# Kernel optimization log

Measured on AMD Instinct MI355X. Metric: run time of the kernel, lower is better.

The kernel has to match this reference:

```python
import jax, jax.numpy as jnp
import numpy as np

B, W, M, H, L, C, LR, RD = 128, 64, 512, 64, 2, 4, 16, 32
D = L * H  # concatenated GRU hidden dim


def setup_inputs() -> dict:
    key = jax.random.key(0)
    ks = jax.random.split(key, 22)
    def rn(k, shape, s=0.1):
        return jax.random.normal(k, shape, jnp.float32) * s
    return dict(
        x=jax.random.normal(ks[0], (B, W, M), jnp.float32),
        H_init=rn(ks[1], (L, M, H)),
        major_graph=rn(ks[2], (M, M), 0.05),
        wx0=rn(ks[3], (3 * H, 1)), wh0=rn(ks[4], (3 * H, H)),
        bx0=rn(ks[5], (3 * H,)), bh0=rn(ks[6], (3 * H,)),
        wx1=rn(ks[7], (3 * H, H)), wh1=rn(ks[8], (3 * H, H)),
        bx1=rn(ks[9], (3 * H,)), bh1=rn(ks[10], (3 * H,)),
        A_v=rn(ks[11], (C, LR, M)), A_g=1.0 + rn(ks[12], (C, LR)), A_b=rn(ks[13], (C, LR)),
        B_v=rn(ks[14], (C, M, LR)), B_g=1.0 + rn(ks[15], (C, M)), B_b=rn(ks[16], (C, M)),
        C_v=rn(ks[17], (C, RD, D)), C_g=1.0 + rn(ks[18], (C, RD)), C_b=rn(ks[19], (C, RD)),
        FR_w=rn(ks[20], (C, M, RD)), FR_b=rn(ks[21], (C, M)),
    )


def _wn(v, g):
    # weight_norm: W = g * v / ||v|| per output row (norm over input dim)
    return g[..., None] * v / jnp.linalg.norm(v, axis=-1, keepdims=True)


def _gru(x, h, wx, wh, bx, bh):
    gx = x @ wx.T + bx            # [B, M, 3H]
    gh = h @ wh.T + bh            # [B, M, 3H]
    xr, xz, xn = jnp.split(gx, 3, axis=-1)
    hr, hz, hn = jnp.split(gh, 3, axis=-1)
    r = jax.nn.sigmoid(xr + hr)
    z = jax.nn.sigmoid(xz + hz)
    n = jnp.tanh(xn + r * hn)
    return n + z * (h - n)


def reference(x, H_init, major_graph, wx0, wh0, bx0, bh0, wx1, wh1, bx1, bh1,
              A_v, A_g, A_b, B_v, B_g, B_b, C_v, C_g, C_b, FR_w, FR_b):
    Bsz = x.shape[0]
    Aw = _wn(A_v, A_g)            # [C, LR, M]
    Bw = _wn(B_v, B_g)            # [C, M, LR]
    Cw = _wn(C_v, C_g)            # [C, RD, D]
    # h0: [L, B, M, H]
    h0 = jnp.broadcast_to(H_init[:, None], (H_init.shape[0], Bsz) + H_init.shape[1:])
    h0_1 = h0[1]

    def step(hn, x_t):
        # NOTE: faithfully, layer0 receives the top layer's hidden from the
        # previous step; layer1 always uses the fixed h0[1].
        h1 = _gru(x_t[..., None], hn, wx0, wh0, bx0, bh0)   # [B, M, H]
        h2 = _gru(h1, h0_1, wx1, wh1, bx1, bh1)             # [B, M, H]
        x_p = jnp.swapaxes(jnp.concatenate([h1, h2], axis=-1), 1, 2)  # [B, D, M]
        x_p0 = jax.nn.relu(x_p @ major_graph)               # [B, D, M]
        a = jnp.einsum('bdm,clm->bcdl', x_p, Aw) + A_b[:, None, :]      # [B,C,D,LR]
        bmid = jnp.einsum('bcdl,cml->bcdm', a, Bw) + B_b[:, None, :]    # [B,C,D,M]
        xr = jax.nn.relu(bmid + x_p0[:, None])              # [B, C, D, M]
        xt = jnp.swapaxes(xr, 2, 3)                         # [B, C, M, D]
        y = jax.nn.sigmoid(jnp.einsum('bcmd,crd->bcmr', xt, Cw) + C_b[:, None, :])
        out = jnp.einsum('bcmr,cmr->bcm', y, FR_w) + FR_b   # [B, C, M]
        return h2, out

    _, outs = jax.lax.scan(step, h0[0], jnp.moveaxis(x, 1, 0))  # [W, B, C, M]
    final = jnp.transpose(outs, (2, 1, 0, 3))                   # [C, B, W, M]
    return final.reshape((-1,) + final.shape[2:])               # [C*B, W, M]
```

## Files before the change

### kernel.cpp

```cpp
#include <hip/hip_runtime.h>
#include <hip/hip_bf16.h>

constexpr int kB  = 128;
constexpr int kW  = 64;
constexpr int kM  = 512;
constexpr int kH  = 64;
constexpr int kC  = 4;
constexpr int kLR = 16;
constexpr int kRD = 32;
constexpr int kD  = 128;
constexpr int kNC = kB * kM;
constexpr int kN  = kM + kC * kLR;

typedef __attribute__((ext_vector_type(8))) short bf16x8;
typedef __attribute__((ext_vector_type(4))) float f32x4;

__device__ __forceinline__ float sigmf(float v) { return 1.f / (1.f + __expf(-v)); }
__device__ __forceinline__ float tanhf2(float v) { float e = __expf(2.f * v); return 1.f - 2.f / (e + 1.f); }

__device__ __forceinline__ unsigned short f2bfu(float f) {
    union { __hip_bfloat16 h; unsigned short u; } cv; cv.h = __float2bfloat16(f); return cv.u;
}
__device__ __forceinline__ float bfu2f(unsigned short s) {
    return __uint_as_float(((unsigned)s) << 16);
}

__device__ __forceinline__ void gl_lds16(const void* g, void* s) {
    __builtin_amdgcn_global_load_lds(
        (const __attribute__((address_space(1))) void*)(g),
        (__attribute__((address_space(3))) void*)(s), 16, 0, 0);
}


__global__ void k_initHc(const float* __restrict__ Hini, __hip_bfloat16* __restrict__ HcG) {
    int id = blockIdx.x * 256 + threadIdx.x;
    int cell = id >> 6, j = id & 63;
    int m = cell & (kM - 1);
    HcG[id] = __float2bfloat16(Hini[m * kH + j]);
}

__global__ void k_h1b(const float* __restrict__ Hini, __hip_bfloat16* __restrict__ H1b) {
    int id = blockIdx.x * 256 + threadIdx.x;
    H1b[id] = __float2bfloat16(Hini[(kM + (id >> 6)) * kH + (id & 63)]);
}

__global__ void k_gh1T(const float* __restrict__ Hini, const float* __restrict__ wh1,
                       const float* __restrict__ bh1, float* __restrict__ gh1T) {
    int id = blockIdx.x * 256 + threadIdx.x;
    int k = id >> 9, m = id & (kM - 1);
    float acc = bh1[k];
    #pragma unroll
    for (int j = 0; j < kH; j++)
        acc = fmaf(Hini[(kM + m) * kH + j], wh1[k * kH + j], acc);
    gh1T[id] = acc;
}

__global__ void k_packW(const float* __restrict__ wh0, const float* __restrict__ wx1,
                        __hip_bfloat16* __restrict__ W0g, __hip_bfloat16* __restrict__ W1x) {
    int id = blockIdx.x * 256 + threadIdx.x;
    W0g[id] = __float2bfloat16(wh0[id]);
    W1x[id] = __float2bfloat16(wx1[id]);
}

__global__ void k_buildGT(const float* __restrict__ G, __hip_bfloat16* __restrict__ BT) {
    int id = blockIdx.x * 256 + threadIdx.x;
    int n = id >> 9, k = id & (kM - 1);
    BT[n * kM + k] = __float2bfloat16(G[k * kM + n]);
}

__global__ void k_norm_aw(const float* __restrict__ Av, const float* __restrict__ Ag,
                          __hip_bfloat16* __restrict__ BT) {
    int row = blockIdx.x;
    int lane = threadIdx.x;
    float v[8]; float s = 0.f;
    #pragma unroll
    for (int q = 0; q < 8; q++) { v[q] = Av[row * kM + q * 64 + lane]; s += v[q] * v[q]; }
    #pragma unroll
    for (int off = 32; off > 0; off >>= 1) s += __shfl_down(s, off);
    s = __shfl(s, 0);
    float scale = Ag[row] / sqrtf(s);
    #pragma unroll
    for (int q = 0; q < 8; q++)
        BT[(kM + row) * kM + q * 64 + lane] = __float2bfloat16(v[q] * scale);
}

__global__ void k_norm_bw(const float* __restrict__ Bv, const float* __restrict__ Bg,
                          const float* __restrict__ Bb, __hip_bfloat16* __restrict__ BwNh) {
    int row = blockIdx.x * 256 + threadIdx.x;
    float v[16]; float s = 0.f;
    #pragma unroll
    for (int l = 0; l < 16; l++) { v[l] = Bv[row * 16 + l]; s += v[l] * v[l]; }
    float scale = Bg[row] / sqrtf(s);
    #pragma unroll
    for (int l = 0; l < 16; l++) BwNh[row * 32 + l] = __float2bfloat16(v[l] * scale);
    BwNh[row * 32 + 16] = __float2bfloat16(Bb[row]);
    #pragma unroll
    for (int l = 17; l < 32; l++) BwNh[row * 32 + l] = __float2bfloat16(0.f);
}

__global__ void k_norm_cw(const float* __restrict__ Cv, const float* __restrict__ Cg,
                          __hip_bfloat16* __restrict__ CwB) {
    int row = blockIdx.x;
    int lane = threadIdx.x;
    float v0 = Cv[row * kD + lane], v1 = Cv[row * kD + 64 + lane];
    float s = v0 * v0 + v1 * v1;
    #pragma unroll
    for (int off = 32; off > 0; off >>= 1) s += __shfl_down(s, off);
    s = __shfl(s, 0);
    float scale = Cg[row] / sqrtf(s);
    CwB[row * kD + lane] = __float2bfloat16(v0 * scale);
    CwB[row * kD + 64 + lane] = __float2bfloat16(v1 * scale);
}

__global__ __launch_bounds__(512) void k_gru(
    const float* __restrict__ x,
    __hip_bfloat16* __restrict__ HcG,
    const __hip_bfloat16* __restrict__ H1b,
    const __hip_bfloat16* __restrict__ W0g,
    const __hip_bfloat16* __restrict__ W1x,
    const float* __restrict__ gh1T,
    const float* __restrict__ wx0, const float* __restrict__ bx0,
    const float* __restrict__ bh0, const float* __restrict__ bx1,
    __hip_bfloat16* __restrict__ XPT, int t)
{
    __shared__ __align__(16) short W0s[192 * 64];
    __shared__ __align__(16) short W1s[192 * 64];
    __shared__ __align__(16) short HlS[128 * 64];
    __shared__ float xsh[128];

    const int tid = threadIdx.x;
    const int blk = blockIdx.x;
    const int w = tid >> 6, lane = tid & 63;
    const int lr = lane & 15, lq = lane >> 4;
    const int b = blk >> 2;
    const int mBlk = (blk & 3) * 128;
    const unsigned short* HcU = (const unsigned short*)HcG;
    const unsigned short* H1U = (const unsigned short*)H1b;
    const size_t cellBase = (size_t)blk * 128;

    #pragma unroll
    for (int it = 0; it < 3; it++) {
        int cid = it * 512 + tid; int row = cid >> 3, c = cid & 7;
        gl_lds16(W0g + row * 64 + ((c ^ (row & 7)) * 8), W0s + cid * 8);
    }
    #pragma unroll
    for (int it = 0; it < 3; it++) {
        int cid = it * 512 + tid; int row = cid >> 3, c = cid & 7;
        gl_lds16(W1x + row * 64 + ((c ^ (row & 7)) * 8), W1s + cid * 8);
    }
    if (tid < 128) xsh[tid] = x[((size_t)b * kW + t) * kM + mBlk + tid];
    __syncthreads();

    const int cl = w * 16 + lr;

    bf16x8 a0[2];
    a0[0] = *(const bf16x8*)&HcU[(cellBase + cl) * 64 + lq * 8];
    a0[1] = *(const bf16x8*)&HcU[(cellBase + cl) * 64 + (4 + lq) * 8];
    f32x4 aR[4] = {}, aZ[4] = {}, aN[4] = {};
    #pragma unroll
    for (int kc = 0; kc < 2; kc++) {
        #pragma unroll
        for (int gt = 0; gt < 4; gt++) {
            const int gR = gt * 16 + lr;
            const int gZ = 64 + gt * 16 + lr;
            const int gN = 128 + gt * 16 + lr;
            bf16x8 bR = *(const bf16x8*)&W0s[gR * 64 + (((kc * 4 + lq) ^ (gR & 7)) * 8)];
            bf16x8 bZ = *(const bf16x8*)&W0s[gZ * 64 + (((kc * 4 + lq) ^ (gZ & 7)) * 8)];
            bf16x8 bN = *(const bf16x8*)&W0s[gN * 64 + (((kc * 4 + lq) ^ (gN & 7)) * 8)];
            aR[gt] = __builtin_amdgcn_mfma_f32_16x16x32_bf16(a0[kc], bR, aR[gt], 0, 0, 0);
            aZ[gt] = __builtin_amdgcn_mfma_f32_16x16x32_bf16(a0[kc], bZ, aZ[gt], 0, 0, 0);
            aN[gt] = __builtin_amdgcn_mfma_f32_16x16x32_bf16(a0[kc], bN, aN[gt], 0, 0, 0);
        }
    }

    #pragma unroll
    for (int gt = 0; gt < 4; gt++) {
        const int i = gt * 16 + lr;
        const float wxr = wx0[i], wxz = wx0[64 + i], wxn = wx0[128 + i];
        const float bsr = bx0[i] + bh0[i];
        const float bsz = bx0[64 + i] + bh0[64 + i];
        const float bxn = bx0[128 + i], bhn = bh0[128 + i];
        unsigned short hu[4];
        #pragma unroll
        for (int r2 = 0; r2 < 4; r2++) {
            const int clr = w * 16 + lq * 4 + r2;
            const float xv = xsh[clr];
            float rr = sigmf(aR[gt][r2] + bsr + xv * wxr);
            float zz = sigmf(aZ[gt][r2] + bsz + xv * wxz);
            float nn = tanhf2(bxn + xv * wxn + rr * (aN[gt][r2] + bhn));
            float hp = bfu2f(HcU[(cellBase + clr) * 64 + i]);
            float h1 = nn + zz * (hp - nn);
            unsigned short u = f2bfu(h1);
            HlS[clr * 64 + (((i >> 3) ^ (clr & 7)) * 8) + (i & 7)] = (short)u;
            hu[r2] = u;
        }
        ushort4 pk; pk.x = hu[0]; pk.y = hu[1]; pk.z = hu[2]; pk.w = hu[3];
        *(ushort4*)((unsigned short*)XPT + (size_t)(b * 128 + i) * kM + mBlk + w * 16 + lq * 4) = pk;
    }

    bf16x8 a1[2];
    a1[0] = *(const bf16x8*)&HlS[cl * 64 + ((lq ^ (cl & 7)) * 8)];
    a1[1] = *(const bf16x8*)&HlS[cl * 64 + (((4 + lq) ^ (cl & 7)) * 8)];
    f32x4 cR[4] = {}, cZ[4] = {}, cN[4] = {};
    #pragma unroll
    for (int kc = 0; kc < 2; kc++) {
        #pragma unroll
        for (int gt = 0; gt < 4; gt++) {
            const int gR = gt * 16 + lr;
            const int gZ = 64 + gt * 16 + lr;
            const int gN = 128 + gt * 16 + lr;
            bf16x8 bR = *(const bf16x8*)&W1s[gR * 64 + (((kc * 4 + lq) ^ (gR & 7)) * 8)];
            bf16x8 bZ = *(const bf16x8*)&W1s[gZ * 64 + (((kc * 4 + lq) ^ (gZ & 7)) * 8)];
            bf16x8 bN = *(const bf16x8*)&W1s[gN * 64 + (((kc * 4 + lq) ^ (gN & 7)) * 8)];
            cR[gt] = __builtin_amdgcn_mfma_f32_16x16x32_bf16(a1[kc], bR, cR[gt], 0, 0, 0);
            cZ[gt] = __builtin_amdgcn_mfma_f32_16x16x32_bf16(a1[kc], bZ, cZ[gt], 0, 0, 0);
            cN[gt] = __builtin_amdgcn_mfma_f32_16x16x32_bf16(a1[kc], bN, cN[gt], 0, 0, 0);
        }
    }

    const int mb4 = mBlk + w * 16 + lq * 4;
    #pragma unroll
    for (int gt = 0; gt < 4; gt++) {
        const int i = gt * 16 + lr;
        const float bxr = bx1[i], bxz = bx1[64 + i], bxn = bx1[128 + i];
        f32x4 gr4 = *(const f32x4*)&gh1T[(size_t)i * kM + mb4];
        f32x4 gz4 = *(const f32x4*)&gh1T[(size_t)(64 + i) * kM + mb4];
        f32x4 gn4 = *(const f32x4*)&gh1T[(size_t)(128 + i) * kM + mb4];
        unsigned short hu[4];
        #pragma unroll
        for (int r2 = 0; r2 < 4; r2++) {
            const int clr = w * 16 + lq * 4 + r2;
            float rr = sigmf(cR[gt][r2] + bxr + gr4[r2]);
            float zz = sigmf(cZ[gt][r2] + bxz + gz4[r2]);
            float nn = tanhf2(cN[gt][r2] + bxn + rr * gn4[r2]);
            float h01 = bfu2f(H1U[(size_t)(mBlk + clr) * 64 + i]);
            float h2 = nn + zz * (h01 - nn);
            unsigned short u = f2bfu(h2);
            hu[r2] = u;
            ((unsigned short*)HcG)[(cellBase + clr) * 64 + i] = u;
        }
        ushort4 pk; pk.x = hu[0]; pk.y = hu[1]; pk.z = hu[2]; pk.w = hu[3];
        *(ushort4*)((unsigned short*)XPT + (size_t)(b * 128 + 64 + i) * kM + mBlk + w * 16 + lq * 4) = pk;
    }
}

__global__ __launch_bounds__(256) void k_tail(
    const __hip_bfloat16* __restrict__ X,
    const __hip_bfloat16* __restrict__ BT,
    const float* __restrict__ Ab,
    const __hip_bfloat16* __restrict__ BwNh,
    const __hip_bfloat16* __restrict__ CwB,
    const float* __restrict__ Cb, const float* __restrict__ FRw,
    const float* __restrict__ FRb, float* __restrict__ OUT, int t)
{
    __shared__ __align__(16) short SM[40960];
    short* xp0L = SM;
    short* aL   = SM + 8192;
    short* Xr   = SM + 32768;

    const int tid = threadIdx.x;
    const int b = blockIdx.x, mseg = blockIdx.y;
    const int w = tid >> 6, lane = tid & 63;
    const int lr = lane & 15, lq = lane >> 4;
    const int wm = w >> 1, wn = w & 1;

    f32x4 acc[4][4] = {};
    const __hip_bfloat16* Xb = X + (size_t)b * 128 * kM;

    auto STAGE = [&](int kk, int buf) {
        short* AsB = SM + buf * 16384;
        short* BsB = AsB + 8192;
        #pragma unroll
        for (int it = 0; it < 4; it++) {
            int cid = it * 256 + tid;
            int row = cid >> 3, ch = cid & 7;
            int cg = ch ^ (row & 7);
            gl_lds16(Xb + (size_t)row * kM + kk + cg * 8, AsB + cid * 8);
        }
        #pragma unroll
        for (int it = 0; it < 4; it++) {
            int cid = it * 256 + tid;
            int j = cid >> 3, ch = cid & 7;
            int cg = ch ^ (j & 7);
            int n = (j < 64) ? (mseg * 64 + j) : (448 + j);
            gl_lds16(BT + (size_t)n * kM + kk + cg * 8, BsB + cid * 8);
        }
    };

    STAGE(0, 0);
    __syncthreads();

    int cur = 0;
    for (int ki = 0; ki < 8; ki++) {
        if (ki < 7) STAGE((ki + 1) * 64, cur ^ 1);
        const short* AsB = SM + cur * 16384;
        const short* BsB = AsB + 8192;
        #pragma unroll
        for (int w2 = 0; w2 < 2; w2++) {
            bf16x8 af[4], bfr[4];
            #pragma unroll
            for (int fi = 0; fi < 4; fi++) {
                int row = wm * 64 + fi * 16 + lr;
                af[fi] = *(const bf16x8*)&AsB[row * 64 + (((w2 * 4 + lq) ^ (row & 7)) * 8)];
            }
            #pragma unroll
            for (int fj = 0; fj < 4; fj++) {
                int col = wn * 64 + fj * 16 + lr;
                bfr[fj] = *(const bf16x8*)&BsB[col * 64 + (((w2 * 4 + lq) ^ (col & 7)) * 8)];
            }
            #pragma unroll
            for (int fi = 0; fi < 4; fi++)
                #pragma unroll
                for (int fj = 0; fj < 4; fj++)
                    acc[fi][fj] = __builtin_amdgcn_mfma_f32_16x16x32_bf16(
                        af[fi], bfr[fj], acc[fi][fj], 0, 0, 0);
        }
        __syncthreads();
        cur ^= 1;
    }

    if (wn == 0) {
        #pragma unroll
        for (int fi = 0; fi < 4; fi++) {
            const int d0 = wm * 64 + fi * 16 + lq * 4;
            const int c16 = d0 >> 3, half = lq & 1;
            #pragma unroll
            for (int fj = 0; fj < 4; fj++) {
                const int ml = fj * 16 + lr;
                unsigned lo = (unsigned)f2bfu(fmaxf(acc[fi][fj][0], 0.f)) |
                              ((unsigned)f2bfu(fmaxf(acc[fi][fj][1], 0.f)) << 16);
                unsigned hi = (unsigned)f2bfu(fmaxf(acc[fi][fj][2], 0.f)) |
                              ((unsigned)f2bfu(fmaxf(acc[fi][fj][3], 0.f)) << 16);
                uint2 pk; pk.x = lo; pk.y = hi;
                *(uint2*)&xp0L[ml * 128 + ((c16 ^ (ml & 7)) * 8) + half * 4] = pk;
            }
        }
    } else {
        #pragma unroll
        for (int fj = 0; fj < 4; fj++) {
            const int clc = fj * 16 + lr;
            const float ab = Ab[clc];
            #pragma unroll
            for (int fi = 0; fi < 4; fi++) {
                #pragma unroll
                for (int r = 0; r < 4; r++) {
                    const int d = wm * 64 + fi * 16 + lq * 4 + r;
                    aL[d * 64 + (((clc >> 3) ^ (d & 7)) * 8) + (clc & 7)] =
                        (short)f2bfu(acc[fi][fj][r] + ab);
                }
            }
        }
    }
    __syncthreads();

    const int c = w;
    bf16x8 af2[8];
    #pragma unroll
    for (int dt = 0; dt < 8; dt++) {
        bf16x8 v = {};
        const int d = dt * 16 + lr;
        if (lq < 2) {
            v = *(const bf16x8*)&aL[d * 64 + (((c * 2 + lq) ^ (d & 7)) * 8)];
        } else if (lq == 2) {
            v[0] = (short)0x3F80;
        }
        af2[dt] = v;
    }
    bf16x8 cwf[2][4];
    #pragma unroll
    for (int rt = 0; rt < 2; rt++)
        #pragma unroll
        for (int s = 0; s < 4; s++)
            cwf[rt][s] = *(const bf16x8*)&CwB[((size_t)(c * kRD + rt * 16 + lr)) * kD + s * 32 + lq * 8];
    const float cbv0 = Cb[c * kRD + lr];
    const float cbv1 = Cb[c * kRD + 16 + lr];
    short* Xrw = Xr + w * 2048;

    for (int mt = 0; mt < 4; mt++) {
        const int mg = mseg * 64 + mt * 16 + lr;
        bf16x8 bf1 = *(const bf16x8*)&BwNh[((size_t)c * kM + mg) * 32 + lq * 8];
        f32x4 acc1[8] = {};
        #pragma unroll
        for (int dt = 0; dt < 8; dt++)
            acc1[dt] = __builtin_amdgcn_mfma_f32_16x16x32_bf16(af2[dt], bf1, acc1[dt], 0, 0, 0);

        const int mlT = mt * 16 + lr;
        #pragma unroll
        for (int dt = 0; dt < 8; dt++) {
            const int c16 = dt * 2 + (lq >> 1), half = lq & 1;
            uint2 xv = *(const uint2*)&xp0L[mlT * 128 + ((c16 ^ (mlT & 7)) * 8) + half * 4];
            float x0 = bfu2f((unsigned short)(xv.x & 0xFFFF));
            float x1 = bfu2f((unsigned short)(xv.x >> 16));
            float x2 = bfu2f((unsigned short)(xv.y & 0xFFFF));
            float x3 = bfu2f((unsigned short)(xv.y >> 16));
            unsigned lo = (unsigned)f2bfu(fmaxf(acc1[dt][0] + x0, 0.f)) |
                          ((unsigned)f2bfu(fmaxf(acc1[dt][1] + x1, 0.f)) << 16);
            unsigned hi = (unsigned)f2bfu(fmaxf(acc1[dt][2] + x2, 0.f)) |
                          ((unsigned)f2bfu(fmaxf(acc1[dt][3] + x3, 0.f)) << 16);
            uint2 pk; pk.x = lo; pk.y = hi;
            *(uint2*)&Xrw[lr * 128 + ((c16 ^ (lr & 7)) * 8) + half * 4] = pk;
        }

        bf16x8 xa[4];
        #pragma unroll
        for (int s = 0; s < 4; s++)
            xa[s] = *(const bf16x8*)&Xrw[lr * 128 + (((s * 4 + lq) ^ (lr & 7)) * 8)];
        float po0 = 0.f, po1 = 0.f, po2 = 0.f, po3 = 0.f;
        const int mrow = mseg * 64 + mt * 16 + lq * 4;
        #pragma unroll
        for (int rt = 0; rt < 2; rt++) {
            f32x4 a2 = {};
            #pragma unroll
            for (int s = 0; s < 4; s++)
                a2 = __builtin_amdgcn_mfma_f32_16x16x32_bf16(xa[s], cwf[rt][s], a2, 0, 0, 0);
            const float cb = rt ? cbv1 : cbv0;
            const int r = rt * 16 + lr;
            po0 = fmaf(sigmf(a2[0] + cb), FRw[((size_t)c * kM + mrow + 0) * kRD + r], po0);
            po1 = fmaf(sigmf(a2[1] + cb), FRw[((size_t)c * kM + mrow + 1) * kRD + r], po1);
            po2 = fmaf(sigmf(a2[2] + cb), FRw[((size_t)c * kM + mrow + 2) * kRD + r], po2);
            po3 = fmaf(sigmf(a2[3] + cb), FRw[((size_t)c * kM + mrow + 3) * kRD + r], po3);
        }
        #pragma unroll
        for (int off = 8; off > 0; off >>= 1) {
            po0 += __shfl_xor(po0, off);
            po1 += __shfl_xor(po1, off);
            po2 += __shfl_xor(po2, off);
            po3 += __shfl_xor(po3, off);
        }
        if (lr == 0) {
            const float* frb = &FRb[c * kM + mrow];
            float4 o;
            o.x = po0 + frb[0]; o.y = po1 + frb[1];
            o.z = po2 + frb[2]; o.w = po3 + frb[3];
            *(float4*)&OUT[((size_t)(c * kB + b) * kW + t) * kM + mrow] = o;
        }
    }
}

extern "C" void kernel_launch(void* const* d_in, const int* in_sizes, int n_in,
                              void* d_out, int out_size, void* d_ws, size_t ws_size,
                              hipStream_t stream) {
    const float* x    = (const float*)d_in[0];
    const float* Hini = (const float*)d_in[1];
    const float* G    = (const float*)d_in[2];
    const float* wx0  = (const float*)d_in[3];
    const float* wh0  = (const float*)d_in[4];
    const float* bx0  = (const float*)d_in[5];
    const float* bh0  = (const float*)d_in[6];
    const float* wx1  = (const float*)d_in[7];
    const float* wh1  = (const float*)d_in[8];
    const float* bx1  = (const float*)d_in[9];
    const float* bh1  = (const float*)d_in[10];
    const float* A_v  = (const float*)d_in[11];
    const float* A_g  = (const float*)d_in[12];
    const float* A_b  = (const float*)d_in[13];
    const float* B_v  = (const float*)d_in[14];
    const float* B_g  = (const float*)d_in[15];
    const float* B_b  = (const float*)d_in[16];
    const float* C_v  = (const float*)d_in[17];
    const float* C_g  = (const float*)d_in[18];
    const float* C_b  = (const float*)d_in[19];
    const float* FR_w = (const float*)d_in[20];
    const float* FR_b = (const float*)d_in[21];
    float* out = (float*)d_out;

    char* w = (char*)d_ws;
    __hip_bfloat16* HcG  = (__hip_bfloat16*)w; w += (size_t)kNC * 64 * 2;
    __hip_bfloat16* XPT  = (__hip_bfloat16*)w; w += (size_t)128 * kNC * 2;
    __hip_bfloat16* BT   = (__hip_bfloat16*)w; w += (size_t)kN * kM * 2;
    __hip_bfloat16* H1b  = (__hip_bfloat16*)w; w += (size_t)kM * kH * 2;
    __hip_bfloat16* W0g  = (__hip_bfloat16*)w; w += (size_t)192 * 64 * 2;
    __hip_bfloat16* W1xg = (__hip_bfloat16*)w; w += (size_t)192 * 64 * 2;
    float*          gh1T = (float*)w;          w += (size_t)192 * kM * 4;
    __hip_bfloat16* BwNh = (__hip_bfloat16*)w; w += (size_t)2048 * 32 * 2;
    __hip_bfloat16* CwB  = (__hip_bfloat16*)w; w += (size_t)kC * kRD * kD * 2;

    k_initHc<<<16384, 256, 0, stream>>>(Hini, HcG);
    k_h1b<<<128, 256, 0, stream>>>(Hini, H1b);
    k_gh1T<<<384, 256, 0, stream>>>(Hini, wh1, bh1, gh1T);
    k_packW<<<48, 256, 0, stream>>>(wh0, wx1, W0g, W1xg);
    k_buildGT<<<1024, 256, 0, stream>>>(G, BT);
    k_norm_aw<<<64, 64, 0, stream>>>(A_v, A_g, BT);
    k_norm_bw<<<8, 256, 0, stream>>>(B_v, B_g, B_b, BwNh);
    k_norm_cw<<<128, 64, 0, stream>>>(C_v, C_g, CwB);

    for (int t = 0; t < kW; t++) {
        k_gru<<<512, 512, 0, stream>>>(x, HcG, H1b, W0g, W1xg, gh1T,
                                       wx0, bx0, bh0, bx1, XPT, t);
        k_tail<<<dim3(128, 8), 256, 0, stream>>>(XPT, BT, A_b, BwNh, CwB,
                                                 C_b, FR_w, FR_b, out, t);
    }
}
```

Before: 3.793 ms.

## Widen k_tail tile to 128 m-columns with 512 threads per block

k_tail now processes 128 m-columns plus the 64 low-rank columns per block using 8 waves (4x2 layout of 64x48 MFMA tiles) instead of 64 m-columns with 4 waves. This halves the grid and amortizes the repeated loading of the X activation tile and the low-rank A columns across twice as many output columns. The second stage splits waves over channel and m-half. k_gru switches to a 2D grid with equivalent indexing. The larger LDS footprint and 512-thread blocks may reduce occupancy.

```diff
diff --git a/kernel.cpp b/kernel.cpp
--- a/kernel.cpp
+++ b/kernel.cpp
@@ -129,14 +129,13 @@
     __shared__ float xsh[128];
 
     const int tid = threadIdx.x;
-    const int blk = blockIdx.x;
     const int w = tid >> 6, lane = tid & 63;
     const int lr = lane & 15, lq = lane >> 4;
-    const int b = blk >> 2;
-    const int mBlk = (blk & 3) * 128;
+    const int b = blockIdx.x;
+    const int mBlk = blockIdx.y * 128;
     const unsigned short* HcU = (const unsigned short*)HcG;
     const unsigned short* H1U = (const unsigned short*)H1b;
-    const size_t cellBase = (size_t)blk * 128;
+    const size_t cellBase = (size_t)b * kM + mBlk;
 
     #pragma unroll
     for (int it = 0; it < 3; it++) {
@@ -244,7 +243,7 @@
     }
 }
 
-__global__ __launch_bounds__(256) void k_tail(
+__global__ __launch_bounds__(512, 4) void k_tail(
     const __hip_bfloat16* __restrict__ X,
     const __hip_bfloat16* __restrict__ BT,
     const float* __restrict__ Ab,
@@ -255,34 +254,34 @@
 {
     __shared__ __align__(16) short SM[40960];
     short* xp0L = SM;
-    short* aL   = SM + 8192;
-    short* Xr   = SM + 32768;
+    short* aL   = SM + 16384;
+    short* Xr   = SM + 24576;
 
     const int tid = threadIdx.x;
     const int b = blockIdx.x, mseg = blockIdx.y;
     const int w = tid >> 6, lane = tid & 63;
     const int lr = lane & 15, lq = lane >> 4;
-    const int wm = w >> 1, wn = w & 1;
-
-    f32x4 acc[4][4] = {};
+    const int wm = w >> 2, wn = w & 3;
+
+    f32x4 acc[4][3] = {};
     const __hip_bfloat16* Xb = X + (size_t)b * 128 * kM;
 
     auto STAGE = [&](int kk, int buf) {
-        short* AsB = SM + buf * 16384;
+        short* AsB = SM + buf * 20480;
         short* BsB = AsB + 8192;
         #pragma unroll
-        for (int it = 0; it < 4; it++) {
-            int cid = it * 256 + tid;
+        for (int it = 0; it < 2; it++) {
+            int cid = it * 512 + tid;
             int row = cid >> 3, ch = cid & 7;
             int cg = ch ^ (row & 7);
             gl_lds16(Xb + (size_t)row * kM + kk + cg * 8, AsB + cid * 8);
         }
         #pragma unroll
-        for (int it = 0; it < 4; it++) {
-            int cid = it * 256 + tid;
+        for (int it = 0; it < 3; it++) {
+            int cid = it * 512 + tid;
             int j = cid >> 3, ch = cid & 7;
             int cg = ch ^ (j & 7);
-            int n = (j < 64) ? (mseg * 64 + j) : (448 + j);
+            int n = (j < 128) ? (mseg * 128 + j) : (384 + j);
             gl_lds16(BT + (size_t)n * kM + kk + cg * 8, BsB + cid * 8);
         }
     };
@@ -293,25 +292,25 @@
     int cur = 0;
     for (int ki = 0; ki < 8; ki++) {
         if (ki < 7) STAGE((ki + 1) * 64, cur ^ 1);
-        const short* AsB = SM + cur * 16384;
+        const short* AsB = SM + cur * 20480;
         const short* BsB = AsB + 8192;
         #pragma unroll
         for (int w2 = 0; w2 < 2; w2++) {
-            bf16x8 af[4], bfr[4];
+            bf16x8 af[4], bfr[3];
             #pragma unroll
             for (int fi = 0; fi < 4; fi++) {
                 int row = wm * 64 + fi * 16 + lr;
                 af[fi] = *(const bf16x8*)&AsB[row * 64 + (((w2 * 4 + lq) ^ (row & 7)) * 8)];
             }
             #pragma unroll
-            for (int fj = 0; fj < 4; fj++) {
-                int col = wn * 64 + fj * 16 + lr;
+            for (int fj = 0; fj < 3; fj++) {
+                int col = wn * 48 + fj * 16 + lr;
                 bfr[fj] = *(const bf16x8*)&BsB[col * 64 + (((w2 * 4 + lq) ^ (col & 7)) * 8)];
             }
             #pragma unroll
             for (int fi = 0; fi < 4; fi++)
                 #pragma unroll
-                for (int fj = 0; fj < 4; fj++)
+                for (int fj = 0; fj < 3; fj++)
                     acc[fi][fj] = __builtin_amdgcn_mfma_f32_16x16x32_bf16(
                         af[fi], bfr[fj], acc[fi][fj], 0, 0, 0);
         }
@@ -319,26 +318,23 @@
         cur ^= 1;
     }
 
-    if (wn == 0) {
-        #pragma unroll
-        for (int fi = 0; fi < 4; fi++) {
-            const int d0 = wm * 64 + fi * 16 + lq * 4;
-            const int c16 = d0 >> 3, half = lq & 1;
-            #pragma unroll
-            for (int fj = 0; fj < 4; fj++) {
-                const int ml = fj * 16 + lr;
+    #pragma unroll
+    for (int fj = 0; fj < 3; fj++) {
+        const int colg = wn * 48 + fj * 16 + lr;
+        if (colg < 128) {
+            #pragma unroll
+            for (int fi = 0; fi < 4; fi++) {
+                const int d0 = wm * 64 + fi * 16 + lq * 4;
+                const int c16 = d0 >> 3, half = lq & 1;
                 unsigned lo = (unsigned)f2bfu(fmaxf(acc[fi][fj][0], 0.f)) |
                               ((unsigned)f2bfu(fmaxf(acc[fi][fj][1], 0.f)) << 16);
                 unsigned hi = (unsigned)f2bfu(fmaxf(acc[fi][fj][2], 0.f)) |
                               ((unsigned)f2bfu(fmaxf(acc[fi][fj][3], 0.f)) << 16);
                 uint2 pk; pk.x = lo; pk.y = hi;
-                *(uint2*)&xp0L[ml * 128 + ((c16 ^ (ml & 7)) * 8) + half * 4] = pk;
+                *(uint2*)&xp0L[colg * 128 + ((c16 ^ (colg & 7)) * 8) + half * 4] = pk;
             }
-        }
-    } else {
-        #pragma unroll
-        for (int fj = 0; fj < 4; fj++) {
-            const int clc = fj * 16 + lr;
+        } else {
+            const int clc = colg - 128;
             const float ab = Ab[clc];
             #pragma unroll
             for (int fi = 0; fi < 4; fi++) {
@@ -353,7 +349,8 @@
     }
     __syncthreads();
 
-    const int c = w;
+    const int c = w & 3;
+    const int mhalf = w >> 2;
     bf16x8 af2[8];
     #pragma unroll
     for (int dt = 0; dt < 8; dt++) {
@@ -377,14 +374,14 @@
     short* Xrw = Xr + w * 2048;
 
     for (int mt = 0; mt < 4; mt++) {
-        const int mg = mseg * 64 + mt * 16 + lr;
+        const int mg = mseg * 128 + mhalf * 64 + mt * 16 + lr;
         bf16x8 bf1 = *(const bf16x8*)&BwNh[((size_t)c * kM + mg) * 32 + lq * 8];
         f32x4 acc1[8] = {};
         #pragma unroll
         for (int dt = 0; dt < 8; dt++)
             acc1[dt] = __builtin_amdgcn_mfma_f32_16x16x32_bf16(af2[dt], bf1, acc1[dt], 0, 0, 0);
 
-        const int mlT = mt * 16 + lr;
+        const int mlT = mhalf * 64 + mt * 16 + lr;
         #pragma unroll
         for (int dt = 0; dt < 8; dt++) {
             const int c16 = dt * 2 + (lq >> 1), half = lq & 1;
@@ -406,7 +403,7 @@
         for (int s = 0; s < 4; s++)
             xa[s] = *(const bf16x8*)&Xrw[lr * 128 + (((s * 4 + lq) ^ (lr & 7)) * 8)];
         float po0 = 0.f, po1 = 0.f, po2 = 0.f, po3 = 0.f;
-        const int mrow = mseg * 64 + mt * 16 + lq * 4;
+        const int mrow = mseg * 128 + mhalf * 64 + mt * 16 + lq * 4;
         #pragma unroll
         for (int rt = 0; rt < 2; rt++) {
             f32x4 a2 = {};
@@ -485,9 +482,9 @@
     k_norm_cw<<<128, 64, 0, stream>>>(C_v, C_g, CwB);
 
     for (int t = 0; t < kW; t++) {
-        k_gru<<<512, 512, 0, stream>>>(x, HcG, H1b, W0g, W1xg, gh1T,
-                                       wx0, bx0, bh0, bx1, XPT, t);
-        k_tail<<<dim3(128, 8), 256, 0, stream>>>(XPT, BT, A_b, BwNh, CwB,
+        k_gru<<<dim3(128, 4), 512, 0, stream>>>(x, HcG, H1b, W0g, W1xg, gh1T,
+                                                wx0, bx0, bh0, bx1, XPT, t);
+        k_tail<<<dim3(128, 4), 512, 0, stream>>>(XPT, BT, A_b, BwNh, CwB,
                                                  C_b, FR_w, FR_b, out, t);
     }
 }
```

Result: faster. 3.146 ms, median of 2 (-17.0%).
